# Performance work log

Measured on AMD Instinct MI355X. Metric: run time of the kernel, lower is better.

The kernel has to match this reference:

```python
import jax, jax.numpy as jnp
import numpy as np

IMG_SIZE = 256
NUM_ANGLES = 360
NUM_DET = 363  # ceil(sqrt(2) * IMG_SIZE)


def setup_inputs() -> dict:
    key = jax.random.key(0)
    sinogram = jax.random.normal(key, (2, 1, NUM_ANGLES, NUM_DET), dtype=jnp.float32)
    return {"sinogram": sinogram}


def _fbp(sinogram):
    B, C, A, D = sinogram.shape
    H = W = IMG_SIZE

    # ---- ramp filter in frequency domain (filter_type='ramp') ----
    freq = jnp.fft.fftfreq(D).astype(jnp.float32)          # (D,)
    filt = 2.0 * jnp.abs(freq)
    sino_fft = jnp.fft.fft(sinogram, axis=-1)
    filtered = jnp.fft.ifft(sino_fft * filt, axis=-1).real.astype(sinogram.dtype)  # (B,C,A,D)

    # ---- backprojection geometry ----
    angles = jnp.linspace(0.0, np.pi * (1.0 - 1.0 / A), A).astype(jnp.float32)  # (A,)
    coords = jnp.linspace(-1.0, 1.0, H).astype(jnp.float32)
    y_grid, x_grid = jnp.meshgrid(coords, coords, indexing='ij')  # (H,W) each

    cos_t = jnp.cos(angles)[:, None, None]  # (A,1,1)
    sin_t = jnp.sin(angles)[:, None, None]
    t = x_grid[None] * cos_t + y_grid[None] * sin_t          # (A,H,W)

    scale = (H - 1) / 2.0 * np.sqrt(2.0) / ((D - 1) / 2.0)
    t_norm = t / scale                                        # normalized grid x in [-1,1]-ish

    # grid_sample, mode='bilinear', padding_mode='zeros', align_corners=True
    # x-coordinate maps to detector index: u = (t_norm + 1)/2 * (D-1)
    u = (t_norm + 1.0) * 0.5 * (D - 1)                        # (A,H,W)
    u0 = jnp.floor(u)
    w1 = u - u0                                               # frac weight for right neighbor
    w0 = 1.0 - w1
    i0 = u0.astype(jnp.int32)
    i1 = i0 + 1
    valid0 = ((i0 >= 0) & (i0 < D)).astype(sinogram.dtype)
    valid1 = ((i1 >= 0) & (i1 < D)).astype(sinogram.dtype)
    i0c = jnp.clip(i0, 0, D - 1)
    i1c = jnp.clip(i1, 0, D - 1)

    HW = H * W
    idx0 = jnp.broadcast_to(i0c.reshape(1, 1, A, HW), (B, C, A, HW))
    idx1 = jnp.broadcast_to(i1c.reshape(1, 1, A, HW), (B, C, A, HW))
    v0 = jnp.take_along_axis(filtered, idx0, axis=-1)         # (B,C,A,HW)
    v1 = jnp.take_along_axis(filtered, idx1, axis=-1)

    w0m = (w0 * valid0).reshape(1, 1, A, HW)
    w1m = (w1 * valid1).reshape(1, 1, A, HW)
    contrib = v0 * w0m + v1 * w1m                             # (B,C,A,HW)

    recon = contrib.sum(axis=2).reshape(B, C, H, W)
    return recon * (np.pi / A)


def reference(sinogram):
    return _fbp(sinogram)
```

## Files before the change

### kernel.cpp

```cpp
#include <hip/hip_runtime.h>
#include <math.h>

#define IMG 256
#define NA  360
#define ND  363
#define NB  2
#define KMAX 181
#define ST  544
#define PAD 76

__global__ __launch_bounds__(384) void fbp_conv(const float* __restrict__ sino,
                                                float* __restrict__ filt) {
    __shared__ float ht[2 * ND - 1];
    const int row = blockIdx.x;
    const int t = threadIdx.x;

    for (int i = t; i < 2 * ND - 1; i += 384) {
        int n = i - (ND - 1);
        double S;
        if (n == 0) {
            S = (double)KMAX * (double)(KMAX + 1) * 0.5;
        } else {
            double w = (2.0 * M_PI / (double)ND) * (double)n;
            S = ((double)(KMAX + 1) * cos((double)KMAX * w)
               - (double)KMAX * cos((double)(KMAX + 1) * w) - 1.0)
              / (2.0 * (1.0 - cos(w)));
        }
        ht[i] = (float)(S * (4.0 / ((double)ND * (double)ND)));
    }
    __syncthreads();

    const float* __restrict__ srow = sino + (size_t)row * ND;
    float* __restrict__ orow = filt + (size_t)row * ST;

    if (t < ND) {
        float acc = 0.f;
#pragma unroll 4
        for (int m = ND - 1; m >= 0; --m) {
            acc = fmaf(srow[m], ht[t + (ND - 1) - m], acc);
        }
        orow[PAD + t] = acc;
    }
    if (t < PAD) orow[t] = 0.f;
    if (t >= PAD && t < PAD + (ST - PAD - ND)) orow[PAD + ND + (t - PAD)] = 0.f;
}

__global__ __launch_bounds__(256) void fbp_backproj(const float* __restrict__ filt,
                                                    float* __restrict__ out,
                                                    float K, float U0p) {
    __shared__ float2 tab[NA];
    const int t = threadIdx.x;
    for (int a = t; a < NA; a += 256) {
        float ang = (float)M_PI * (float)a / (float)NA;
        float s, c;
        sincosf(ang, &s, &c);
        tab[a] = make_float2(c * K, s * K);
    }
    __syncthreads();

    const int blk   = blockIdx.x;
    const int chunk = blk >> 8;
    const int pb    = blk & 255;
    const int gid   = pb * 256 + t;
    const int img   = gid >> 15;
    const int rest  = gid & 32767;
    const int iy    = rest >> 8;
    const int jx    = rest & 255;

    const float xg = -1.f + 2.f * (float)jx / 255.f;
    const float yg = -1.f + 2.f * (float)iy / 255.f;
    const float DY = 2.f * 128.f / 255.f;

    const float* __restrict__ base = filt + (size_t)img * NA * ST;
    float acc0 = 0.f, acc1 = 0.f;
    const int a0 = chunk * (NA / 8);

#pragma unroll 5
    for (int a = a0; a < a0 + NA / 8; ++a) {
        float2 cs = tab[a];
        float u0 = fmaf(xg, cs.x, fmaf(yg, cs.y, U0p));
        float u1 = fmaf(DY, cs.y, u0);
        float f0 = floorf(u0);
        float f1 = floorf(u1);
        int   i0 = (int)f0;
        int   i1 = (int)f1;
        float w0 = u0 - f0;
        float w1 = u1 - f1;
        const float* rp = base + a * ST;
        float v0 = (1.f - w0) * rp[i0];
        v0 = fmaf(w0, rp[i0 + 1], v0);
        float v1 = (1.f - w1) * rp[i1];
        v1 = fmaf(w1, rp[i1 + 1], v1);
        acc0 += v0;
        acc1 += v1;
    }

    const float SCL = (float)M_PI / (float)NA;
    const int p0 = img * 65536 + iy * 256 + jx;
    atomicAdd(out + p0,                 acc0 * SCL);
    atomicAdd(out + p0 + 128 * 256,     acc1 * SCL);
}

extern "C" void kernel_launch(void* const* d_in, const int* in_sizes, int n_in,
                              void* d_out, int out_size, void* d_ws, size_t ws_size,
                              hipStream_t stream) {
    const float* sino = (const float*)d_in[0];
    float* out = (float*)d_out;
    float* filt = (float*)d_ws;

    const double scale = (double)(IMG - 1) / 2.0 * sqrt(2.0) / ((double)(ND - 1) / 2.0);
    const float  K   = (float)(0.5 * (double)(ND - 1) / scale);
    const float  U0p = 0.5f * (float)(ND - 1) + (float)PAD;

    fbp_conv<<<NB * NA, 384, 0, stream>>>(sino, filt);
    hipMemsetAsync(d_out, 0, (size_t)out_size * sizeof(float), stream);
    fbp_backproj<<<8 * 256, 256, 0, stream>>>(filt, out, K, U0p);
}
```

Measured before the change: 98.15 us.

## Split angles across waves in a block and reduce in shared memory

Backprojection now gives each block 64 pixels of one row, and its four waves each take a quarter of the angles. Partial sums are combined in shared memory and written directly, which removes the output memset and the global atomics. The old scheme gave each thread two pixels sharing one angle table read. That reuse is dropped, so per-angle trig setup is repeated more often. A launch-bounds occupancy hint is added.

```diff
diff --git a/kernel.cpp b/kernel.cpp
--- a/kernel.cpp
+++ b/kernel.cpp
@@ -45,10 +45,11 @@
     if (t >= PAD && t < PAD + (ST - PAD - ND)) orow[PAD + ND + (t - PAD)] = 0.f;
 }
 
-__global__ __launch_bounds__(256) void fbp_backproj(const float* __restrict__ filt,
-                                                    float* __restrict__ out,
-                                                    float K, float U0p) {
+__global__ __launch_bounds__(256, 8) void fbp_backproj(const float* __restrict__ filt,
+                                                       float* __restrict__ out,
+                                                       float K, float U0p) {
     __shared__ float2 tab[NA];
+    __shared__ float  part[256];
     const int t = threadIdx.x;
     for (int a = t; a < NA; a += 256) {
         float ang = (float)M_PI * (float)a / (float)NA;
@@ -58,47 +59,39 @@
     }
     __syncthreads();
 
-    const int blk   = blockIdx.x;
-    const int chunk = blk >> 8;
-    const int pb    = blk & 255;
-    const int gid   = pb * 256 + t;
-    const int img   = gid >> 15;
-    const int rest  = gid & 32767;
-    const int iy    = rest >> 8;
-    const int jx    = rest & 255;
+    const int blk  = blockIdx.x;
+    const int img  = blk >> 10;
+    const int iy   = (blk >> 2) & 255;
+    const int jx0  = (blk & 3) * 64;
+    const int lane = t & 63;
+    const int wv   = t >> 6;
 
-    const float xg = -1.f + 2.f * (float)jx / 255.f;
+    const float xg = -1.f + 2.f * (float)(jx0 + lane) / 255.f;
     const float yg = -1.f + 2.f * (float)iy / 255.f;
-    const float DY = 2.f * 128.f / 255.f;
 
     const float* __restrict__ base = filt + (size_t)img * NA * ST;
-    float acc0 = 0.f, acc1 = 0.f;
-    const int a0 = chunk * (NA / 8);
+    float acc = 0.f;
+    const int a0 = wv * (NA / 4);
 
-#pragma unroll 5
-    for (int a = a0; a < a0 + NA / 8; ++a) {
+#pragma unroll 6
+    for (int a = a0; a < a0 + NA / 4; ++a) {
         float2 cs = tab[a];
-        float u0 = fmaf(xg, cs.x, fmaf(yg, cs.y, U0p));
-        float u1 = fmaf(DY, cs.y, u0);
-        float f0 = floorf(u0);
-        float f1 = floorf(u1);
-        int   i0 = (int)f0;
-        int   i1 = (int)f1;
-        float w0 = u0 - f0;
-        float w1 = u1 - f1;
+        float u  = fmaf(xg, cs.x, fmaf(yg, cs.y, U0p));
+        float uf = floorf(u);
+        int   i0 = (int)uf;
+        float w1 = u - uf;
         const float* rp = base + a * ST;
-        float v0 = (1.f - w0) * rp[i0];
-        v0 = fmaf(w0, rp[i0 + 1], v0);
-        float v1 = (1.f - w1) * rp[i1];
-        v1 = fmaf(w1, rp[i1 + 1], v1);
-        acc0 += v0;
-        acc1 += v1;
+        float v = (1.f - w1) * rp[i0];
+        acc += fmaf(w1, rp[i0 + 1], v);
     }
 
-    const float SCL = (float)M_PI / (float)NA;
-    const int p0 = img * 65536 + iy * 256 + jx;
-    atomicAdd(out + p0,                 acc0 * SCL);
-    atomicAdd(out + p0 + 128 * 256,     acc1 * SCL);
+    part[t] = acc;
+    __syncthreads();
+
+    if (t < 64) {
+        float s = part[t] + part[t + 64] + part[t + 128] + part[t + 192];
+        out[img * 65536 + iy * 256 + jx0 + t] = s * ((float)M_PI / (float)NA);
+    }
 }
 
 extern "C" void kernel_launch(void* const* d_in, const int* in_sizes, int n_in,
@@ -113,6 +106,5 @@
     const float  U0p = 0.5f * (float)(ND - 1) + (float)PAD;
 
     fbp_conv<<<NB * NA, 384, 0, stream>>>(sino, filt);
-    hipMemsetAsync(d_out, 0, (size_t)out_size * sizeof(float), stream);
-    fbp_backproj<<<8 * 256, 256, 0, stream>>>(filt, out, K, U0p);
+    fbp_backproj<<<2048, 256, 0, stream>>>(filt, out, K, U0p);
 }
```

Result: no change. 97.36 us (-0.8%).
